# Kernel optimization log

Hardware: AMD Instinct MI355X
Metric: run time of the kernel (lower is better)

## Reference

```python
import jax, jax.numpy as jnp
import numpy as np

B, K, S, H = 8, 2048, 1024, 256   # batch, num_spans, seq_len, hidden
W = 24                            # max span width (gather window)
WIN = 3
NEG_INF = -jnp.inf


def setup_inputs() -> dict:
    key = jax.random.key(0)
    k1, k2, k3, k4 = jax.random.split(key, 4)
    token_reps = jax.random.normal(k1, (B, S, H), dtype=jnp.float32)
    starts = jax.random.randint(k2, (B, K), 0, S - W)
    widths = jax.random.randint(k3, (B, K), 1, W + 1)  # span width in [1, W]
    ends = starts + widths                              # end is exclusive, <= S
    span_ids = jnp.stack([starts, ends], axis=-1).astype(jnp.int32)
    span_masks = jax.random.uniform(k4, (B, K)) < 0.9
    return {"token_reps": token_reps, "span_ids": span_ids, "span_masks": span_masks}


def _masked_max(tok_win, mask):
    # tok_win: (B, K, W, H), mask: (B, K, W) -> (B, K, H)
    return jnp.max(jnp.where(mask[..., None], tok_win, NEG_INF), axis=2)


def reference(token_reps, span_ids, span_masks):
    """extract_span_reps, mode='start_inner_maxpool_end', pooling=False.

    Equivalent math to the torch version, but gathers only the per-span window
    [start, start+W) instead of broadcasting over the full seq_len, since all
    spans have width <= W.
    """
    Bv, Sv, Hv = token_reps.shape
    starts = span_ids[..., 0]            # (B, K)
    ends = span_ids[..., 1]              # (B, K) exclusive

    pos = jnp.arange(W)                  # (W,)
    idx = starts[..., None] + pos        # (B, K, W) absolute token index
    safe_idx = jnp.clip(idx, 0, Sv - 1)  # safe gather; out-of-span masked below
    # gather per-span token windows: (B, K, W, H)
    tok_win = token_reps[jnp.arange(Bv)[:, None, None], safe_idx]

    valid = span_masks[..., None]                                 # (B, K, 1)
    start_cut = jnp.minimum(starts + WIN, ends)[..., None]        # (B, K, 1)
    end_cut = jnp.maximum(ends - WIN, starts)[..., None]          # (B, K, 1)
    e = ends[..., None]

    # idx >= start always holds (pos >= 0)
    start_m = (idx < start_cut) & valid
    end_m = (idx >= end_cut) & (idx < e) & valid
    inner_m = ((idx >= start_cut) & (idx < end_cut)
               & ((ends - starts) > 2 * WIN)[..., None] & valid)

    start_reps = _masked_max(tok_win, start_m)   # (B, K, H)
    end_reps = _masked_max(tok_win, end_m)
    inner_reps = _masked_max(tok_win, inner_m)

    # spans with no inner tokens fall back to start reps
    no_inner = jnp.isinf(inner_reps).all(axis=-1, keepdims=True)
    inner_reps = jnp.where(no_inner, start_reps, inner_reps)

    span_reps = jnp.concatenate([start_reps, inner_reps, end_reps], axis=-1)
    span_reps = jnp.where(span_masks[..., None], span_reps, 0.0)  # (B, K, 3H)
    return span_reps
```

## Files before the change

### kernel.cpp

```cpp
#include <hip/hip_runtime.h>

#define Bv   8
#define Kv   2048
#define Sv   1024
#define Hv   256
#define Wv   24
#define WINv 3

#define NSPAN (Bv * Kv)

typedef float f32x4 __attribute__((ext_vector_type(4)));

__device__ __forceinline__ float bf16_to_f32(unsigned short u) {
    union { unsigned int i; float f; } c;
    c.i = ((unsigned int)u) << 16;
    return c.f;
}

__device__ __forceinline__ void nt_store4(f32x4* p, float a, float b, float c, float d) {
    f32x4 v = { a, b, c, d };
    __builtin_nontemporal_store(v, p);
}

__global__ __launch_bounds__(512) void span_rep_kernel(
    const void* __restrict__ token_reps,
    const int* __restrict__ span_ids,
    const void* __restrict__ span_masks,
    float* __restrict__ out)
{
    __shared__ int s_tok32;
    __shared__ int s_ids64;
    __shared__ int s_maskw;

    const int tid = threadIdx.x;
    if (tid < 64) {
        const unsigned short* tu = (const unsigned short*)token_reps;
        int e = (tu[2 * tid] >> 7) & 0xFF;
        unsigned long long votes = __ballot(e >= 96 && e <= 144);

        const unsigned char* mb = (const unsigned char*)span_masks;
        unsigned char bnz = mb[tid] | mb[tid + 64];
        int m4 = tid & 3;
        unsigned long long z1  = __ballot(bnz && m4 == 1);
        unsigned long long z23 = __ballot(bnz && (m4 == 2 || m4 == 3));
        unsigned long long z84 = __ballot(bnz && m4 == 0 && (tid & 7) == 4);

        if (tid == 0) {
            s_tok32 = (__popcll(votes) >= 56) ? 0 : 1;
            s_maskw = z1 ? 0 : (z23 ? 3 : (z84 ? 1 : 2));
            int odd_or = span_ids[1] | span_ids[3] | span_ids[5] | span_ids[7];
            s_ids64 = (odd_or == 0) ? 1 : 0;
        }
    }
    __syncthreads();

    const int b    = blockIdx.x & 7;
    const int k    = ((blockIdx.x >> 3) << 3) + (tid >> 6);
    const int span = b * Kv + k;
    const int lane = tid & 63;

    f32x4* out4 = (f32x4*)(out + (size_t)span * (3 * Hv)) + lane;

    int mv;
    if (s_maskw == 0)      mv = ((const unsigned char*)span_masks)[span];
    else if (s_maskw == 1) mv = ((const int*)span_masks)[span];
    else if (s_maskw == 2) mv = ((const int*)span_masks)[2 * span];
    else                   mv = (((const float*)span_masks)[span] != 0.0f);

    int start, end;
    if (!s_ids64) {
        start = span_ids[2 * span];
        end   = span_ids[2 * span + 1];
    } else {
        start = span_ids[4 * span];
        end   = span_ids[4 * span + 2];
    }
    const int w = end - start;

    if (mv == 0 || w < 1 || w > Wv || start < 0 || end > Sv) {
        nt_store4(out4,          0.f, 0.f, 0.f, 0.f);
        nt_store4(out4 + Hv / 4, 0.f, 0.f, 0.f, 0.f);
        nt_store4(out4 + Hv / 2, 0.f, 0.f, 0.f, 0.f);
        return;
    }

    const size_t row0 = ((size_t)b * Sv + start) * Hv;

    float s0 = -INFINITY, s1 = -INFINITY, s2 = -INFINITY, s3 = -INFINITY;
    float e0 = -INFINITY, e1 = -INFINITY, e2 = -INFINITY, e3 = -INFINITY;
    float i0 = -INFINITY, i1 = -INFINITY, i2 = -INFINITY, i3 = -INFINITY;

    const int  scut      = (w < WINv) ? w : WINv;
    const int  ecut      = (w - WINv > 0) ? (w - WINv) : 0;
    const bool has_inner = (w > 2 * WINv);
    const int  icut      = w - WINv;

    if (s_tok32) {
        const float* bp = (const float*)token_reps + row0 + lane * 4;
        float4 buf[Wv];
        #pragma unroll
        for (int j = 0; j < Wv; ++j)
            if (j < w) buf[j] = *(const float4*)(bp + j * Hv);
        #pragma unroll
        for (int j = 0; j < Wv; ++j) {
            if (j < w) {
                float4 f = buf[j];
                if (j < scut) {
                    s0 = fmaxf(s0, f.x); s1 = fmaxf(s1, f.y);
                    s2 = fmaxf(s2, f.z); s3 = fmaxf(s3, f.w);
                }
                if (j >= ecut) {
                    e0 = fmaxf(e0, f.x); e1 = fmaxf(e1, f.y);
                    e2 = fmaxf(e2, f.z); e3 = fmaxf(e3, f.w);
                }
                if (has_inner && j >= WINv && j < icut) {
                    i0 = fmaxf(i0, f.x); i1 = fmaxf(i1, f.y);
                    i2 = fmaxf(i2, f.z); i3 = fmaxf(i3, f.w);
                }
            }
        }
    } else {
        const unsigned short* bp = (const unsigned short*)token_reps + row0 + lane * 4;
        ushort4 buf[Wv];
        #pragma unroll
        for (int j = 0; j < Wv; ++j)
            if (j < w) buf[j] = *(const ushort4*)(bp + j * Hv);
        #pragma unroll
        for (int j = 0; j < Wv; ++j) {
            if (j < w) {
                float f0 = bf16_to_f32(buf[j].x), f1 = bf16_to_f32(buf[j].y);
                float f2 = bf16_to_f32(buf[j].z), f3 = bf16_to_f32(buf[j].w);
                if (j < scut) {
                    s0 = fmaxf(s0, f0); s1 = fmaxf(s1, f1);
                    s2 = fmaxf(s2, f2); s3 = fmaxf(s3, f3);
                }
                if (j >= ecut) {
                    e0 = fmaxf(e0, f0); e1 = fmaxf(e1, f1);
                    e2 = fmaxf(e2, f2); e3 = fmaxf(e3, f3);
                }
                if (has_inner && j >= WINv && j < icut) {
                    i0 = fmaxf(i0, f0); i1 = fmaxf(i1, f1);
                    i2 = fmaxf(i2, f2); i3 = fmaxf(i3, f3);
                }
            }
        }
    }
    if (!has_inner) { i0 = s0; i1 = s1; i2 = s2; i3 = s3; }

    nt_store4(out4,          s0, s1, s2, s3);
    nt_store4(out4 + Hv / 4, i0, i1, i2, i3);
    nt_store4(out4 + Hv / 2, e0, e1, e2, e3);
}

extern "C" void kernel_launch(void* const* d_in, const int* in_sizes, int n_in,
                              void* d_out, int out_size, void* d_ws, size_t ws_size,
                              hipStream_t stream) {
    const void* token_reps = d_in[0];
    const int*  span_ids   = (const int*)d_in[1];
    const void* span_masks = d_in[2];
    for (int i = 0; i < n_in; ++i) {
        if (in_sizes[i] == Bv * Sv * Hv)      token_reps = d_in[i];
        else if (in_sizes[i] == Bv * Kv * 2)  span_ids   = (const int*)d_in[i];
        else if (in_sizes[i] == Bv * Kv)      span_masks = d_in[i];
    }
    float* out = (float*)d_out;

    dim3 grid(NSPAN / 8);
    dim3 block(512);
    span_rep_kernel<<<grid, block, 0, stream>>>(token_reps, span_ids, span_masks, out);
}
```

Baseline: 90.73 us.

## Split span gather into start/end/inner chunks, make scalars uniform, halve block size

Replaces the single 24-row register buffer with separate small start and end window loads and a chunked loop over inner rows, so each row is loaded once per segment and fewer registers are held live. This should raise occupancy. Span bounds and the mask are made wave-uniform with readfirstlane so branches become scalar. Blocks shrink to 256 threads (4 spans each) with twice as many blocks. The inner chunk loop adds a runtime loop with partial-chunk predication, and the start and end windows can overlap, so a few rows may be read twice.

```diff
diff --git a/kernel.cpp b/kernel.cpp
--- a/kernel.cpp
+++ b/kernel.cpp
@@ -6,23 +6,28 @@
 #define Hv   256
 #define Wv   24
 #define WINv 3
+#define RBI  9
 
 #define NSPAN (Bv * Kv)
 
 typedef float f32x4 __attribute__((ext_vector_type(4)));
-
-__device__ __forceinline__ float bf16_to_f32(unsigned short u) {
-    union { unsigned int i; float f; } c;
-    c.i = ((unsigned int)u) << 16;
-    return c.f;
-}
 
 __device__ __forceinline__ void nt_store4(f32x4* p, float a, float b, float c, float d) {
     f32x4 v = { a, b, c, d };
     __builtin_nontemporal_store(v, p);
 }
 
-__global__ __launch_bounds__(512) void span_rep_kernel(
+__device__ __forceinline__ void bf16x4_to_f32(uint2 u, float& f0, float& f1,
+                                              float& f2, float& f3) {
+    union { unsigned i; float f; } a, b, c, d;
+    a.i = u.x << 16;
+    b.i = u.x & 0xFFFF0000u;
+    c.i = u.y << 16;
+    d.i = u.y & 0xFFFF0000u;
+    f0 = a.f; f1 = b.f; f2 = c.f; f3 = d.f;
+}
+
+__global__ __launch_bounds__(256) void span_rep_kernel(
     const void* __restrict__ token_reps,
     const int* __restrict__ span_ids,
     const void* __restrict__ span_masks,
@@ -55,7 +60,7 @@
     __syncthreads();
 
     const int b    = blockIdx.x & 7;
-    const int k    = ((blockIdx.x >> 3) << 3) + (tid >> 6);
+    const int k    = ((blockIdx.x >> 3) << 2) + (tid >> 6);
     const int span = b * Kv + k;
     const int lane = tid & 63;
 
@@ -75,6 +80,10 @@
         start = span_ids[4 * span];
         end   = span_ids[4 * span + 2];
     }
+
+    start = __builtin_amdgcn_readfirstlane(start);
+    end   = __builtin_amdgcn_readfirstlane(end);
+    mv    = __builtin_amdgcn_readfirstlane(mv);
     const int w = end - start;
 
     if (mv == 0 || w < 1 || w > Wv || start < 0 || end > Sv) {
@@ -84,64 +93,102 @@
         return;
     }
 
+    const int  scut      = (w < WINv) ? w : WINv;
+    const int  ecut      = (w > WINv) ? (w - WINv) : 0;
+    const int  ec        = w - ecut;
+    const bool has_inner = (w > 2 * WINv);
+    const int  icut      = w - WINv;
+
     const size_t row0 = ((size_t)b * Sv + start) * Hv;
 
     float s0 = -INFINITY, s1 = -INFINITY, s2 = -INFINITY, s3 = -INFINITY;
     float e0 = -INFINITY, e1 = -INFINITY, e2 = -INFINITY, e3 = -INFINITY;
     float i0 = -INFINITY, i1 = -INFINITY, i2 = -INFINITY, i3 = -INFINITY;
 
-    const int  scut      = (w < WINv) ? w : WINv;
-    const int  ecut      = (w - WINv > 0) ? (w - WINv) : 0;
-    const bool has_inner = (w > 2 * WINv);
-    const int  icut      = w - WINv;
-
     if (s_tok32) {
         const float* bp = (const float*)token_reps + row0 + lane * 4;
-        float4 buf[Wv];
-        #pragma unroll
-        for (int j = 0; j < Wv; ++j)
-            if (j < w) buf[j] = *(const float4*)(bp + j * Hv);
-        #pragma unroll
-        for (int j = 0; j < Wv; ++j) {
-            if (j < w) {
-                float4 f = buf[j];
-                if (j < scut) {
-                    s0 = fmaxf(s0, f.x); s1 = fmaxf(s1, f.y);
-                    s2 = fmaxf(s2, f.z); s3 = fmaxf(s3, f.w);
-                }
-                if (j >= ecut) {
-                    e0 = fmaxf(e0, f.x); e1 = fmaxf(e1, f.y);
-                    e2 = fmaxf(e2, f.z); e3 = fmaxf(e3, f.w);
-                }
-                if (has_inner && j >= WINv && j < icut) {
-                    i0 = fmaxf(i0, f.x); i1 = fmaxf(i1, f.y);
-                    i2 = fmaxf(i2, f.z); i3 = fmaxf(i3, f.w);
-                }
+        const float* ep = bp + (size_t)ecut * Hv;
+
+        float4 sb[WINv], eb[WINv];
+        #pragma unroll
+        for (int j = 0; j < WINv; ++j)
+            if (j < scut) sb[j] = *(const float4*)(bp + j * Hv);
+        #pragma unroll
+        for (int j = 0; j < WINv; ++j)
+            if (j < ec)   eb[j] = *(const float4*)(ep + j * Hv);
+        #pragma unroll
+        for (int j = 0; j < WINv; ++j)
+            if (j < scut) {
+                s0 = fmaxf(s0, sb[j].x); s1 = fmaxf(s1, sb[j].y);
+                s2 = fmaxf(s2, sb[j].z); s3 = fmaxf(s3, sb[j].w);
+            }
+        #pragma unroll
+        for (int j = 0; j < WINv; ++j)
+            if (j < ec) {
+                e0 = fmaxf(e0, eb[j].x); e1 = fmaxf(e1, eb[j].y);
+                e2 = fmaxf(e2, eb[j].z); e3 = fmaxf(e3, eb[j].w);
+            }
+
+        if (has_inner) {
+            const float* ip = bp + WINv * Hv;
+            for (int r0 = WINv; r0 < icut; r0 += RBI, ip += RBI * Hv) {
+                const int n = ((icut - r0) < RBI) ? (icut - r0) : RBI;
+                float4 buf[RBI];
+                #pragma unroll
+                for (int j = 0; j < RBI; ++j)
+                    if (j < n) buf[j] = *(const float4*)(ip + j * Hv);
+                #pragma unroll
+                for (int j = 0; j < RBI; ++j)
+                    if (j < n) {
+                        i0 = fmaxf(i0, buf[j].x); i1 = fmaxf(i1, buf[j].y);
+                        i2 = fmaxf(i2, buf[j].z); i3 = fmaxf(i3, buf[j].w);
+                    }
             }
         }
     } else {
         const unsigned short* bp = (const unsigned short*)token_reps + row0 + lane * 4;
-        ushort4 buf[Wv];
-        #pragma unroll
-        for (int j = 0; j < Wv; ++j)
-            if (j < w) buf[j] = *(const ushort4*)(bp + j * Hv);
-        #pragma unroll
-        for (int j = 0; j < Wv; ++j) {
-            if (j < w) {
-                float f0 = bf16_to_f32(buf[j].x), f1 = bf16_to_f32(buf[j].y);
-                float f2 = bf16_to_f32(buf[j].z), f3 = bf16_to_f32(buf[j].w);
-                if (j < scut) {
-                    s0 = fmaxf(s0, f0); s1 = fmaxf(s1, f1);
-                    s2 = fmaxf(s2, f2); s3 = fmaxf(s3, f3);
-                }
-                if (j >= ecut) {
-                    e0 = fmaxf(e0, f0); e1 = fmaxf(e1, f1);
-                    e2 = fmaxf(e2, f2); e3 = fmaxf(e3, f3);
-                }
-                if (has_inner && j >= WINv && j < icut) {
-                    i0 = fmaxf(i0, f0); i1 = fmaxf(i1, f1);
-                    i2 = fmaxf(i2, f2); i3 = fmaxf(i3, f3);
-                }
+        const unsigned short* ep = bp + (size_t)ecut * Hv;
+
+        uint2 sb[WINv], eb[WINv];
+        #pragma unroll
+        for (int j = 0; j < WINv; ++j)
+            if (j < scut) sb[j] = *(const uint2*)(bp + j * Hv);
+        #pragma unroll
+        for (int j = 0; j < WINv; ++j)
+            if (j < ec)   eb[j] = *(const uint2*)(ep + j * Hv);
+        #pragma unroll
+        for (int j = 0; j < WINv; ++j)
+            if (j < scut) {
+                float f0, f1, f2, f3;
+                bf16x4_to_f32(sb[j], f0, f1, f2, f3);
+                s0 = fmaxf(s0, f0); s1 = fmaxf(s1, f1);
+                s2 = fmaxf(s2, f2); s3 = fmaxf(s3, f3);
+            }
+        #pragma unroll
+        for (int j = 0; j < WINv; ++j)
+            if (j < ec) {
+                float f0, f1, f2, f3;
+                bf16x4_to_f32(eb[j], f0, f1, f2, f3);
+                e0 = fmaxf(e0, f0); e1 = fmaxf(e1, f1);
+                e2 = fmaxf(e2, f2); e3 = fmaxf(e3, f3);
+            }
+
+        if (has_inner) {
+            const unsigned short* ip = bp + WINv * Hv;
+            for (int r0 = WINv; r0 < icut; r0 += RBI, ip += RBI * Hv) {
+                const int n = ((icut - r0) < RBI) ? (icut - r0) : RBI;
+                uint2 buf[RBI];
+                #pragma unroll
+                for (int j = 0; j < RBI; ++j)
+                    if (j < n) buf[j] = *(const uint2*)(ip + j * Hv);
+                #pragma unroll
+                for (int j = 0; j < RBI; ++j)
+                    if (j < n) {
+                        float f0, f1, f2, f3;
+                        bf16x4_to_f32(buf[j], f0, f1, f2, f3);
+                        i0 = fmaxf(i0, f0); i1 = fmaxf(i1, f1);
+                        i2 = fmaxf(i2, f2); i3 = fmaxf(i3, f3);
+                    }
             }
         }
     }
@@ -165,7 +212,7 @@
     }
     float* out = (float*)d_out;
 
-    dim3 grid(NSPAN / 8);
-    dim3 block(512);
+    dim3 grid(NSPAN / 4);
+    dim3 block(256);
     span_rep_kernel<<<grid, block, 0, stream>>>(token_reps, span_ids, span_masks, out);
 }
```

New measurement: 88.64 us. -2.3%, faster.
